# Optimization experiments

Measured on AMD Instinct MI355X. Metric: run time of the kernel, lower is better.

The kernel has to match this reference:

```python
import jax, jax.numpy as jnp
import numpy as np

N = 12288      # num nodes == in_num_dim (num_center_nodes)
D_IN = 512     # in_node_dim
D_EMB = 128    # embed_dim
D_OUT = 64     # out_dim
E = 393216     # num edges (avg degree 32)
NEG_SLOPE = 0.2  # GATConv default negative_slope


def _glorot(k, shape):
    lim = float(np.sqrt(6.0 / (shape[0] + shape[1])))
    return jax.random.uniform(k, shape, jnp.float32, -lim, lim)


def setup_inputs() -> dict:
    key = jax.random.key(0)
    ks = jax.random.split(key, 13)
    x = jax.random.normal(ks[0], (N, D_IN), jnp.float32)
    edge_index = jax.random.randint(ks[1], (2, E), 0, N, jnp.int64)
    # StructureAE.dense: Linear(in_node_dim, embed_dim)
    W_s1 = _glorot(ks[2], (D_EMB, D_IN))
    b_s1 = jnp.zeros((D_EMB,), jnp.float32)
    # GATConv(embed_dim, out_dim): heads=1, concat, bias
    W_g = _glorot(ks[3], (D_OUT, D_EMB))
    a_src = _glorot(ks[4], (D_OUT, 1))[:, 0]
    a_dst = _glorot(ks[5], (D_OUT, 1))[:, 0]
    b_g = jnp.zeros((D_OUT,), jnp.float32)
    # AttributeAE: dense1 = Linear(N, embed_dim), dense2 = Linear(embed_dim, out_dim)
    W_a1 = _glorot(ks[6], (D_EMB, N))
    b_a1 = jnp.zeros((D_EMB,), jnp.float32)
    W_a2 = _glorot(ks[7], (D_OUT, D_EMB))
    b_a2 = jnp.zeros((D_OUT,), jnp.float32)
    return dict(x=x, W_s1=W_s1, b_s1=b_s1, W_g=W_g, a_src=a_src, a_dst=a_dst,
                b_g=b_g, W_a1=W_a1, b_a1=b_a1, W_a2=W_a2, b_a2=b_a2,
                edge_index=edge_index, batch_size=N)


def _gat(x1, W_g, a_src, a_dst, b_g, edge_index):
    """Single-head GATConv with self-loops (PyG defaults)."""
    n = x1.shape[0]
    g = x1 @ W_g.T                                   # [N, D_OUT]
    loops = jnp.arange(n, dtype=edge_index.dtype)
    src = jnp.concatenate([edge_index[0], loops])    # message source j
    dst = jnp.concatenate([edge_index[1], loops])    # message target i
    sc_src = g @ a_src                               # [N]
    sc_dst = g @ a_dst                               # [N]
    e = jax.nn.leaky_relu(sc_src[src] + sc_dst[dst], NEG_SLOPE)  # [E+N]
    m = jax.ops.segment_max(e, dst, num_segments=n)
    e = jnp.exp(e - m[dst])
    denom = jax.ops.segment_sum(e, dst, num_segments=n)
    alpha = e / denom[dst]                           # softmax per target node
    h = jax.ops.segment_sum(alpha[:, None] * g[src], dst, num_segments=n)
    return h + b_g


def reference(x, W_s1, b_s1, W_g, a_src, a_dst, b_g,
              W_a1, b_a1, W_a2, b_a2, edge_index, batch_size):
    n = x.shape[0]
    # StructureAE (dropout=0 -> identity)
    x1 = jax.nn.relu(x @ W_s1.T + b_s1)              # [N, D_EMB]
    h = _gat(x1, W_g, a_src, a_dst, b_g, edge_index)  # [N, D_OUT]
    s_ = jax.nn.sigmoid(h @ h.T)                     # [N, N]
    # AttributeAE on x[:num_center_nodes] (pad if batch smaller)
    xp = x if batch_size >= n else jnp.pad(x, ((0, n - batch_size), (0, 0)))
    xt = jax.nn.relu(xp.T @ W_a1.T + b_a1)           # [D_IN, D_EMB]
    xa = xt @ W_a2.T + b_a2                          # [D_IN, D_OUT]
    x_ = h @ xa.T                                    # [N, D_IN]
    return (x_, s_)
```

## Files before the change

kernel.cpp:

```cpp
#include <hip/hip_runtime.h>
#include <cstddef>
#include <cstdint>

#define N_NODES 12288
#define D_IN    512
#define D_EMB   128
#define D_OUT   64
#define NEDGE   393216

typedef __attribute__((ext_vector_type(8))) short short8;
typedef __attribute__((ext_vector_type(4))) float f32x4;

__device__ __forceinline__ ushort f2bf(float f) {
  uint32_t u = __float_as_uint(f);
  u += 0x7fffu + ((u >> 16) & 1u);
  return (ushort)(u >> 16);
}
__device__ __forceinline__ float bf2f(ushort h) {
  return __uint_as_float((uint32_t)h << 16);
}

__global__ __launch_bounds__(256) void conv_hilo(const float* __restrict__ src,
    ushort* __restrict__ hi, ushort* __restrict__ lo)
{
  int idx = (blockIdx.x * 256 + threadIdx.x) * 4;
  float4 v = *(const float4*)(src + idx);
  const float* pv = &v.x;
  ushort4 h, l;
  ushort* ph = &h.x; ushort* pl = &l.x;
#pragma unroll
  for (int q = 0; q < 4; ++q) {
    ph[q] = f2bf(pv[q]);
    pl[q] = f2bf(pv[q] - bf2f(ph[q]));
  }
  *(ushort4*)(hi + idx) = h;
  *(ushort4*)(lo + idx) = l;
}

__global__ __launch_bounds__(256) void conv_x(const float* __restrict__ x,
    ushort* __restrict__ xhi, ushort* __restrict__ xlo,
    ushort* __restrict__ xThi, ushort* __restrict__ xTlo)
{
  __shared__ float t4[64][68];
  int i0 = blockIdx.x * 64, c0 = blockIdx.y * 64;
  int ty = threadIdx.x >> 2;
  int tx = threadIdx.x & 3;
#pragma unroll
  for (int p = 0; p < 4; ++p) {
    int col = (tx + p * 4) * 4;
    float4 v = *(const float4*)(x + (size_t)(i0 + ty) * D_IN + c0 + col);
    const float* pv = &v.x;
    ushort4 h, l;
    ushort* ph = &h.x; ushort* pl = &l.x;
#pragma unroll
    for (int q = 0; q < 4; ++q) {
      ph[q] = f2bf(pv[q]);
      pl[q] = f2bf(pv[q] - bf2f(ph[q]));
      t4[col + q][ty] = pv[q];
    }
    size_t o = (size_t)(i0 + ty) * D_IN + c0 + col;
    *(ushort4*)(xhi + o) = h;
    *(ushort4*)(xlo + o) = l;
  }
  __syncthreads();
  int cy = threadIdx.x >> 2;
  int cx = threadIdx.x & 3;
#pragma unroll
  for (int g4 = 0; g4 < 4; ++g4) {
    float4 w = *(const float4*)&t4[cy][cx * 16 + g4 * 4];
    const float* pw = &w.x;
    ushort4 th, tl;
    ushort* pth = &th.x; ushort* ptl = &tl.x;
#pragma unroll
    for (int q = 0; q < 4; ++q) {
      pth[q] = f2bf(pw[q]);
      ptl[q] = f2bf(pw[q] - bf2f(pth[q]));
    }
    size_t ot = (size_t)(c0 + cy) * N_NODES + i0 + cx * 16 + g4 * 4;
    *(ushort4*)(xThi + ot) = th;
    *(ushort4*)(xTlo + ot) = tl;
  }
}

__global__ __launch_bounds__(256) void init_kernel(const int* __restrict__ ei,
    int* __restrict__ flag, int* __restrict__ deg)
{
  int idx = blockIdx.x * 256 + threadIdx.x;
  if (idx < N_NODES) deg[idx] = 0;
  if (idx == 0) {
    int ok = 1;
    for (int t = 0; t < 64; ++t) ok &= (ei[2 * t + 1] == 0);
    *flag = ok;
  }
}

__global__ __launch_bounds__(256) void edge_deg(const int* __restrict__ ei,
    const int* __restrict__ flag, int* __restrict__ deg)
{
  int e = blockIdx.x * 256 + threadIdx.x;
  if (e >= NEDGE) return;
  int dst = (*flag) ? ei[2 * (NEDGE + e)] : ei[NEDGE + e];
  atomicAdd(&deg[dst], 1);
}

__global__ __launch_bounds__(256) void scan_deg(const int* __restrict__ deg,
    int* __restrict__ rp, int* __restrict__ cursor)
{
  __shared__ int sums[256];
  constexpr int C = N_NODES / 256;
  int t = threadIdx.x;
  int base = t * C;
  int local[C];
  int s = 0;
  for (int i = 0; i < C; ++i) { local[i] = deg[base + i]; s += local[i]; }
  sums[t] = s;
  __syncthreads();
  for (int off = 1; off < 256; off <<= 1) {
    int v = (t >= off) ? sums[t - off] : 0;
    __syncthreads();
    sums[t] += v;
    __syncthreads();
  }
  int prefix = (t == 0) ? 0 : sums[t - 1];
  for (int i = 0; i < C; ++i) {
    rp[base + i] = prefix;
    cursor[base + i] = prefix;
    prefix += local[i];
  }
  if (t == 255) rp[N_NODES] = prefix;
}

__global__ __launch_bounds__(256) void edge_scatter(const int* __restrict__ ei,
    const int* __restrict__ flag, int* __restrict__ cursor, int* __restrict__ csr)
{
  int e = blockIdx.x * 256 + threadIdx.x;
  if (e >= NEDGE) return;
  int is64 = *flag;
  int src = is64 ? ei[2 * e] : ei[e];
  int dst = is64 ? ei[2 * (NEDGE + e)] : ei[NEDGE + e];
  int p = atomicAdd(&cursor[dst], 1);
  csr[p] = src;
}

template<int WY, int WX, int MODE>
__global__ __launch_bounds__(256) void mfma_nt(
    const ushort* __restrict__ Ahi, const ushort* __restrict__ Alo,
    const ushort* __restrict__ Bhi, const ushort* __restrict__ Blo,
    const float* __restrict__ bias,
    float* __restrict__ Cf, ushort* __restrict__ Chi, ushort* __restrict__ Clo,
    int lda, int ldb, int K, int ldc, size_t part_stride)
{
  int lane = threadIdx.x & 63;
  int wave = threadIdx.x >> 6;
  int wy = wave / WX, wx = wave % WX;
  int i0 = blockIdx.x * (64 * WY) + wy * 64;
  int j0 = blockIdx.y * (64 * WX) + wx * 64;
  int kbase = blockIdx.z * K;
  float* Cout = Cf + (size_t)blockIdx.z * part_stride;
  int lm = lane & 15, lk = lane >> 4;
  f32x4 acc[4][4];
#pragma unroll
  for (int r = 0; r < 4; ++r)
#pragma unroll
    for (int c = 0; c < 4; ++c) acc[r][c] = (f32x4){0.f, 0.f, 0.f, 0.f};

  for (int k0 = 0; k0 < K; k0 += 32) {
    int kk = kbase + k0 + lk * 8;
    short8 Ah[4], Al[4], Bh[4], Bl[4];
#pragma unroll
    for (int t = 0; t < 4; ++t) {
      size_t ra = (size_t)(i0 + t * 16 + lm) * lda + kk;
      size_t rb = (size_t)(j0 + t * 16 + lm) * ldb + kk;
      Ah[t] = *(const short8*)(Ahi + ra);
      Al[t] = *(const short8*)(Alo + ra);
      Bh[t] = *(const short8*)(Bhi + rb);
      Bl[t] = *(const short8*)(Blo + rb);
    }
#pragma unroll
    for (int r = 0; r < 4; ++r)
#pragma unroll
      for (int c = 0; c < 4; ++c) {
        acc[r][c] = __builtin_amdgcn_mfma_f32_16x16x32_bf16(Ah[r], Bh[c], acc[r][c], 0, 0, 0);
        acc[r][c] = __builtin_amdgcn_mfma_f32_16x16x32_bf16(Ah[r], Bl[c], acc[r][c], 0, 0, 0);
        acc[r][c] = __builtin_amdgcn_mfma_f32_16x16x32_bf16(Al[r], Bh[c], acc[r][c], 0, 0, 0);
      }
  }
#pragma unroll
  for (int r = 0; r < 4; ++r)
#pragma unroll
    for (int c = 0; c < 4; ++c) {
      int col = j0 + c * 16 + lm;
#pragma unroll
      for (int q = 0; q < 4; ++q) {
        int row = i0 + r * 16 + lk * 4 + q;
        float v = acc[r][c][q];
        if (MODE == 0) {
          Cout[(size_t)row * ldc + col] = v;
        } else {
          v += bias[col];
          v = fmaxf(v, 0.f);
          ushort hb = f2bf(v);
          Chi[(size_t)row * ldc + col] = hb;
          Clo[(size_t)row * ldc + col] = f2bf(v - bf2f(hb));
        }
      }
    }
}

template<int ACT>
__global__ __launch_bounds__(256) void gemm_nt64(const float* __restrict__ A,
    const float* __restrict__ B, const float* __restrict__ bias,
    float* __restrict__ C, int M, int N, int K, int ldc)
{
  __shared__ float As[32][64];
  __shared__ float Bs[32][64];
  int m0 = blockIdx.x * 64, n0 = blockIdx.y * 64;
  int tid = threadIdx.x;
  int tx = tid & 15, ty = tid >> 4;
  float acc[4][4] = {};
  for (int k0 = 0; k0 < K; k0 += 32) {
#pragma unroll
    for (int p = 0; p < 2; ++p) {
      int idx = tid + p * 256;
      int row = idx >> 3;
      int kq  = idx & 7;
      float4 va = *(const float4*)(A + (size_t)(m0 + row) * K + k0 + kq * 4);
      As[kq*4+0][row] = va.x; As[kq*4+1][row] = va.y;
      As[kq*4+2][row] = va.z; As[kq*4+3][row] = va.w;
      float4 vb = *(const float4*)(B + (size_t)(n0 + row) * K + k0 + kq * 4);
      Bs[kq*4+0][row] = vb.x; Bs[kq*4+1][row] = vb.y;
      Bs[kq*4+2][row] = vb.z; Bs[kq*4+3][row] = vb.w;
    }
    __syncthreads();
#pragma unroll
    for (int k = 0; k < 32; ++k) {
      float a[4], b[4];
      *(float4*)a = *(const float4*)&As[k][ty * 4];
      *(float4*)b = *(const float4*)&Bs[k][tx * 4];
#pragma unroll
      for (int r = 0; r < 4; ++r)
#pragma unroll
        for (int c = 0; c < 4; ++c)
          acc[r][c] = fmaf(a[r], b[c], acc[r][c]);
    }
    __syncthreads();
  }
#pragma unroll
  for (int r = 0; r < 4; ++r) {
    int m = m0 + ty * 4 + r;
    float4 o;
    float* po = &o.x;
#pragma unroll
    for (int c = 0; c < 4; ++c) {
      float v = acc[r][c];
      if (bias) v += bias[n0 + tx * 4 + c];
      if (ACT) v = fmaxf(v, 0.f);
      po[c] = v;
    }
    *(float4*)(C + (size_t)m * ldc + n0 + tx * 4) = o;
  }
}

__global__ __launch_bounds__(256) void scores_kernel(const float* __restrict__ g,
    const float* __restrict__ a_src, const float* __restrict__ a_dst,
    float* __restrict__ sc_s, float* __restrict__ sc_d)
{
  int lane = threadIdx.x & 63;
  int i = blockIdx.x * 4 + (threadIdx.x >> 6);
  float gv = g[(size_t)i * 64 + lane];
  float vs = gv * a_src[lane];
  float vd = gv * a_dst[lane];
#pragma unroll
  for (int off = 32; off; off >>= 1) {
    vs += __shfl_xor(vs, off);
    vd += __shfl_xor(vd, off);
  }
  if (lane == 0) { sc_s[i] = vs; sc_d[i] = vd; }
}

__global__ __launch_bounds__(256) void gat_kernel(const int* __restrict__ rp,
    const int* __restrict__ csr, const float* __restrict__ sc_s,
    const float* __restrict__ sc_d, const float* __restrict__ g,
    const float* __restrict__ b_g,
    ushort* __restrict__ hhi, ushort* __restrict__ hlo)
{
  int lane = threadIdx.x & 63;
  int i = blockIdx.x * 4 + (threadIdx.x >> 6);
  int beg = rp[i], end = rp[i + 1];
  int deg = end - beg;
  float scd = sc_d[i];
  float mymax = -3.4e38f;
  for (int j = lane; j <= deg; j += 64) {
    int s = (j < deg) ? csr[beg + j] : i;
    float e = sc_s[s] + scd;
    e = (e > 0.f) ? e : 0.2f * e;
    mymax = fmaxf(mymax, e);
  }
#pragma unroll
  for (int off = 32; off; off >>= 1) mymax = fmaxf(mymax, __shfl_xor(mymax, off));
  float sum = 0.f;
  for (int j = lane; j <= deg; j += 64) {
    int s = (j < deg) ? csr[beg + j] : i;
    float e = sc_s[s] + scd;
    e = (e > 0.f) ? e : 0.2f * e;
    sum += __expf(e - mymax);
  }
#pragma unroll
  for (int off = 32; off; off >>= 1) sum += __shfl_xor(sum, off);
  float inv = 1.f / sum;
  float acc = 0.f;
  for (int j = 0; j <= deg; ++j) {
    int s = (j < deg) ? csr[beg + j] : i;
    float e = sc_s[s] + scd;
    e = (e > 0.f) ? e : 0.2f * e;
    float w = __expf(e - mymax) * inv;
    acc = fmaf(w, g[(size_t)s * 64 + lane], acc);
  }
  float val = acc + b_g[lane];
  size_t o = (size_t)i * 64 + lane;
  ushort hi = f2bf(val);
  hhi[o] = hi;
  hlo[o] = f2bf(val - bf2f(hi));
}

__global__ __launch_bounds__(256) void xt_ep(const float* __restrict__ part,
    const float* __restrict__ b_a1, float* __restrict__ xt)
{
  int idx = blockIdx.x * 256 + threadIdx.x;
  float v = b_a1[idx & 127];
#pragma unroll 8
  for (int c = 0; c < 32; ++c) v += part[(size_t)c * (D_IN * D_EMB) + idx];
  xt[idx] = fmaxf(v, 0.f);
}

__global__ __launch_bounds__(256) void sig_hht_mfma(const ushort* __restrict__ hhi,
    const ushort* __restrict__ hlo, float* __restrict__ out)
{
  int lane = threadIdx.x & 63;
  int wave = threadIdx.x >> 6;
  int i0 = blockIdx.x * 128 + (wave >> 1) * 64;
  int j0 = blockIdx.y * 128 + (wave & 1) * 64;
  int lm = lane & 15, lk = lane >> 4;
  f32x4 acc[4][4];
#pragma unroll
  for (int r = 0; r < 4; ++r)
#pragma unroll
    for (int c = 0; c < 4; ++c) acc[r][c] = (f32x4){0.f, 0.f, 0.f, 0.f};
#pragma unroll
  for (int ks = 0; ks < 2; ++ks) {
    short8 Ah[4], Al[4], Bh[4], Bl[4];
#pragma unroll
    for (int t = 0; t < 4; ++t) {
      size_t ra = (size_t)(i0 + t * 16 + lm) * 64 + ks * 32 + lk * 8;
      size_t rb = (size_t)(j0 + t * 16 + lm) * 64 + ks * 32 + lk * 8;
      Ah[t] = *(const short8*)(hhi + ra);
      Al[t] = *(const short8*)(hlo + ra);
      Bh[t] = *(const short8*)(hhi + rb);
      Bl[t] = *(const short8*)(hlo + rb);
    }
#pragma unroll
    for (int r = 0; r < 4; ++r)
#pragma unroll
      for (int c = 0; c < 4; ++c) {
        acc[r][c] = __builtin_amdgcn_mfma_f32_16x16x32_bf16(Ah[r], Bh[c], acc[r][c], 0, 0, 0);
        acc[r][c] = __builtin_amdgcn_mfma_f32_16x16x32_bf16(Ah[r], Bl[c], acc[r][c], 0, 0, 0);
        acc[r][c] = __builtin_amdgcn_mfma_f32_16x16x32_bf16(Al[r], Bh[c], acc[r][c], 0, 0, 0);
      }
  }
#pragma unroll
  for (int r = 0; r < 4; ++r)
#pragma unroll
    for (int c = 0; c < 4; ++c) {
#pragma unroll
      for (int q = 0; q < 4; ++q) {
        float v = acc[r][c][q];
        float ex = __expf(-v);
        float s = 1.f / (1.f + ex);
        out[(size_t)(i0 + r * 16 + lk * 4 + q) * N_NODES + (j0 + c * 16 + lm)] = s;
      }
    }
}

extern "C" void kernel_launch(void* const* d_in, const int* in_sizes, int n_in,
                              void* d_out, int out_size, void* d_ws, size_t ws_size,
                              hipStream_t stream)
{
  const float* x     = (const float*)d_in[0];
  const float* W_s1  = (const float*)d_in[1];
  const float* b_s1  = (const float*)d_in[2];
  const float* W_g   = (const float*)d_in[3];
  const float* a_src = (const float*)d_in[4];
  const float* a_dst = (const float*)d_in[5];
  const float* b_g   = (const float*)d_in[6];
  const float* W_a1  = (const float*)d_in[7];
  const float* b_a1  = (const float*)d_in[8];
  const float* W_a2  = (const float*)d_in[9];
  const float* b_a2  = (const float*)d_in[10];
  const int*   ei    = (const int*)d_in[11];

  float* ws   = (float*)d_ws;
  float* g    = ws;
  float* sc_s = g + (size_t)N_NODES * D_OUT;
  float* sc_d = sc_s + N_NODES;
  float* part = sc_d + N_NODES;
  float* xt   = part + (size_t)32 * D_IN * D_EMB;
  float* xa   = xt + D_IN * D_EMB;
  int* ip     = (int*)(xa + D_IN * D_OUT);
  int* flag   = ip;
  int* deg    = ip + 64;
  int* rp     = deg + N_NODES;
  int* cursor = rp + 12352;
  int* csr    = cursor + N_NODES;
  ushort* up  = (ushort*)(csr + NEDGE);
  ushort* xhi  = up;                         up += (size_t)N_NODES * D_IN;
  ushort* xlo  = up;                         up += (size_t)N_NODES * D_IN;
  ushort* xThi = up;                         up += (size_t)N_NODES * D_IN;
  ushort* xTlo = up;                         up += (size_t)N_NODES * D_IN;
  ushort* x1hi = up;                         up += (size_t)N_NODES * D_EMB;
  ushort* x1lo = up;                         up += (size_t)N_NODES * D_EMB;
  ushort* Ws1hi = up;                        up += (size_t)D_EMB * D_IN;
  ushort* Ws1lo = up;                        up += (size_t)D_EMB * D_IN;
  ushort* Wghi = up;                         up += (size_t)D_OUT * D_EMB;
  ushort* Wglo = up;                         up += (size_t)D_OUT * D_EMB;
  ushort* Wa1hi = up;                        up += (size_t)D_EMB * N_NODES;
  ushort* Wa1lo = up;                        up += (size_t)D_EMB * N_NODES;
  ushort* hhi = up;                          up += (size_t)N_NODES * D_OUT;
  ushort* hlo = up;                          up += (size_t)N_NODES * D_OUT;
  ushort* xahi = up;                         up += (size_t)D_IN * D_OUT;
  ushort* xalo = up;                         up += (size_t)D_IN * D_OUT;

  float* out_x = (float*)d_out;
  float* out_s = out_x + (size_t)N_NODES * D_IN;

  conv_x<<<dim3(192, 8), 256, 0, stream>>>(x, xhi, xlo, xThi, xTlo);
  conv_hilo<<<(D_EMB * D_IN) / 1024, 256, 0, stream>>>(W_s1, Ws1hi, Ws1lo);
  conv_hilo<<<(D_OUT * D_EMB) / 1024, 256, 0, stream>>>(W_g, Wghi, Wglo);
  conv_hilo<<<((size_t)D_EMB * N_NODES) / 1024, 256, 0, stream>>>(W_a1, Wa1hi, Wa1lo);

  init_kernel<<<48, 256, 0, stream>>>(ei, flag, deg);
  edge_deg<<<NEDGE / 256, 256, 0, stream>>>(ei, flag, deg);
  scan_deg<<<1, 256, 0, stream>>>(deg, rp, cursor);
  edge_scatter<<<NEDGE / 256, 256, 0, stream>>>(ei, flag, cursor, csr);

  mfma_nt<2, 2, 1><<<dim3(96, 1, 1), 256, 0, stream>>>(
      xhi, xlo, Ws1hi, Ws1lo, b_s1, nullptr, x1hi, x1lo,
      D_IN, D_IN, D_IN, D_EMB, 0);
  mfma_nt<4, 1, 0><<<dim3(48, 1, 1), 256, 0, stream>>>(
      x1hi, x1lo, Wghi, Wglo, nullptr, g, nullptr, nullptr,
      D_EMB, D_EMB, D_EMB, D_OUT, 0);
  scores_kernel<<<N_NODES / 4, 256, 0, stream>>>(g, a_src, a_dst, sc_s, sc_d);
  gat_kernel<<<N_NODES / 4, 256, 0, stream>>>(rp, csr, sc_s, sc_d, g, b_g,
                                              hhi, hlo);

  mfma_nt<2, 2, 0><<<dim3(4, 1, 32), 256, 0, stream>>>(
      xThi, xTlo, Wa1hi, Wa1lo, nullptr, part, nullptr, nullptr,
      N_NODES, N_NODES, 384, D_EMB, (size_t)D_IN * D_EMB);
  xt_ep<<<D_IN * D_EMB / 256, 256, 0, stream>>>(part, b_a1, xt);
  gemm_nt64<0><<<dim3(8, 1), 256, 0, stream>>>(xt, W_a2, b_a2, xa,
                                               D_IN, D_OUT, D_EMB, D_OUT);
  conv_hilo<<<(D_IN * D_OUT) / 1024, 256, 0, stream>>>(xa, xahi, xalo);

  mfma_nt<2, 2, 0><<<dim3(96, 4, 1), 256, 0, stream>>>(
      hhi, hlo, xahi, xalo, nullptr, out_x, nullptr, nullptr,
      D_OUT, D_OUT, D_OUT, D_IN, 0);
  sig_hht_mfma<<<dim3(96, 96), 256, 0, stream>>>(hhi, hlo, out_s);
}
```

Before: 969.5 us.

## Drop transposed x and W_a1 conversion, use FP32 split-K SIMT, cache GAT weights

Removes the transposed bf16 hi/lo copy of x and the hi/lo conversion of W_a1. The x^T·W_a1^T product is now computed directly from fp32 inputs with a shared-memory split-K SIMT kernel over 64 partitions, with a larger reduction in the epilogue. Small weight conversions are merged into one launch. The MFMA GEMMs switch to single-wave 64-thread blocks on a larger grid. The GAT kernel caches neighbor indices and exp weights in LDS so the third pass skips recomputation. The trade is less conversion traffic and fewer launches against slower non-MFMA FP32 arithmetic for the big reduction GEMM.

```diff
diff --git a/kernel.cpp b/kernel.cpp
--- a/kernel.cpp
+++ b/kernel.cpp
@@ -37,49 +37,25 @@
   *(ushort4*)(lo + idx) = l;
 }
 
-__global__ __launch_bounds__(256) void conv_x(const float* __restrict__ x,
-    ushort* __restrict__ xhi, ushort* __restrict__ xlo,
-    ushort* __restrict__ xThi, ushort* __restrict__ xTlo)
-{
-  __shared__ float t4[64][68];
-  int i0 = blockIdx.x * 64, c0 = blockIdx.y * 64;
-  int ty = threadIdx.x >> 2;
-  int tx = threadIdx.x & 3;
-#pragma unroll
-  for (int p = 0; p < 4; ++p) {
-    int col = (tx + p * 4) * 4;
-    float4 v = *(const float4*)(x + (size_t)(i0 + ty) * D_IN + c0 + col);
-    const float* pv = &v.x;
-    ushort4 h, l;
-    ushort* ph = &h.x; ushort* pl = &l.x;
-#pragma unroll
-    for (int q = 0; q < 4; ++q) {
-      ph[q] = f2bf(pv[q]);
-      pl[q] = f2bf(pv[q] - bf2f(ph[q]));
-      t4[col + q][ty] = pv[q];
-    }
-    size_t o = (size_t)(i0 + ty) * D_IN + c0 + col;
-    *(ushort4*)(xhi + o) = h;
-    *(ushort4*)(xlo + o) = l;
-  }
-  __syncthreads();
-  int cy = threadIdx.x >> 2;
-  int cx = threadIdx.x & 3;
-#pragma unroll
-  for (int g4 = 0; g4 < 4; ++g4) {
-    float4 w = *(const float4*)&t4[cy][cx * 16 + g4 * 4];
-    const float* pw = &w.x;
-    ushort4 th, tl;
-    ushort* pth = &th.x; ushort* ptl = &tl.x;
-#pragma unroll
-    for (int q = 0; q < 4; ++q) {
-      pth[q] = f2bf(pw[q]);
-      ptl[q] = f2bf(pw[q] - bf2f(pth[q]));
-    }
-    size_t ot = (size_t)(c0 + cy) * N_NODES + i0 + cx * 16 + g4 * 4;
-    *(ushort4*)(xThi + ot) = th;
-    *(ushort4*)(xTlo + ot) = tl;
-  }
+__global__ __launch_bounds__(256) void conv_w(const float* __restrict__ Ws1,
+    const float* __restrict__ Wg, ushort* __restrict__ s1h, ushort* __restrict__ s1l,
+    ushort* __restrict__ wgh, ushort* __restrict__ wgl)
+{
+  int b = blockIdx.x;
+  const float* src; ushort* hi; ushort* lo; int idx;
+  if (b < 64) { src = Ws1; hi = s1h; lo = s1l; idx = (b * 256 + threadIdx.x) * 4; }
+  else        { src = Wg;  hi = wgh; lo = wgl; idx = ((b - 64) * 256 + threadIdx.x) * 4; }
+  float4 v = *(const float4*)(src + idx);
+  const float* pv = &v.x;
+  ushort4 h, l;
+  ushort* ph = &h.x; ushort* pl = &l.x;
+#pragma unroll
+  for (int q = 0; q < 4; ++q) {
+    ph[q] = f2bf(pv[q]);
+    pl[q] = f2bf(pv[q] - bf2f(ph[q]));
+  }
+  *(ushort4*)(hi + idx) = h;
+  *(ushort4*)(lo + idx) = l;
 }
 
 __global__ __launch_bounds__(256) void init_kernel(const int* __restrict__ ei,
@@ -142,21 +118,17 @@
   csr[p] = src;
 }
 
-template<int WY, int WX, int MODE>
-__global__ __launch_bounds__(256) void mfma_nt(
+template<int MODE>
+__global__ __launch_bounds__(64) void mfma_nt1(
     const ushort* __restrict__ Ahi, const ushort* __restrict__ Alo,
     const ushort* __restrict__ Bhi, const ushort* __restrict__ Blo,
     const float* __restrict__ bias,
     float* __restrict__ Cf, ushort* __restrict__ Chi, ushort* __restrict__ Clo,
-    int lda, int ldb, int K, int ldc, size_t part_stride)
-{
-  int lane = threadIdx.x & 63;
-  int wave = threadIdx.x >> 6;
-  int wy = wave / WX, wx = wave % WX;
-  int i0 = blockIdx.x * (64 * WY) + wy * 64;
-  int j0 = blockIdx.y * (64 * WX) + wx * 64;
-  int kbase = blockIdx.z * K;
-  float* Cout = Cf + (size_t)blockIdx.z * part_stride;
+    int lda, int ldb, int K, int ldc)
+{
+  int lane = threadIdx.x;
+  int i0 = blockIdx.x * 64;
+  int j0 = blockIdx.y * 64;
   int lm = lane & 15, lk = lane >> 4;
   f32x4 acc[4][4];
 #pragma unroll
@@ -165,7 +137,7 @@
     for (int c = 0; c < 4; ++c) acc[r][c] = (f32x4){0.f, 0.f, 0.f, 0.f};
 
   for (int k0 = 0; k0 < K; k0 += 32) {
-    int kk = kbase + k0 + lk * 8;
+    int kk = k0 + lk * 8;
     short8 Ah[4], Al[4], Bh[4], Bl[4];
 #pragma unroll
     for (int t = 0; t < 4; ++t) {
@@ -195,7 +167,7 @@
         int row = i0 + r * 16 + lk * 4 + q;
         float v = acc[r][c][q];
         if (MODE == 0) {
-          Cout[(size_t)row * ldc + col] = v;
+          Cf[(size_t)row * ldc + col] = v;
         } else {
           v += bias[col];
           v = fmaxf(v, 0.f);
@@ -278,14 +250,18 @@
   if (lane == 0) { sc_s[i] = vs; sc_d[i] = vd; }
 }
 
+#define WCAP 192
 __global__ __launch_bounds__(256) void gat_kernel(const int* __restrict__ rp,
     const int* __restrict__ csr, const float* __restrict__ sc_s,
     const float* __restrict__ sc_d, const float* __restrict__ g,
     const float* __restrict__ b_g,
     ushort* __restrict__ hhi, ushort* __restrict__ hlo)
 {
+  __shared__ float wbuf[4][WCAP];
+  __shared__ int   sbuf[4][WCAP];
   int lane = threadIdx.x & 63;
-  int i = blockIdx.x * 4 + (threadIdx.x >> 6);
+  int w = threadIdx.x >> 6;
+  int i = blockIdx.x * 4 + w;
   int beg = rp[i], end = rp[i + 1];
   int deg = end - beg;
   float scd = sc_d[i];
@@ -295,26 +271,33 @@
     float e = sc_s[s] + scd;
     e = (e > 0.f) ? e : 0.2f * e;
     mymax = fmaxf(mymax, e);
+    if (j < WCAP) sbuf[w][j] = s;
   }
 #pragma unroll
   for (int off = 32; off; off >>= 1) mymax = fmaxf(mymax, __shfl_xor(mymax, off));
   float sum = 0.f;
   for (int j = lane; j <= deg; j += 64) {
-    int s = (j < deg) ? csr[beg + j] : i;
+    int s = (j < WCAP) ? sbuf[w][j] : ((j < deg) ? csr[beg + j] : i);
     float e = sc_s[s] + scd;
     e = (e > 0.f) ? e : 0.2f * e;
-    sum += __expf(e - mymax);
+    float ex = __expf(e - mymax);
+    sum += ex;
+    if (j < WCAP) wbuf[w][j] = ex;
   }
 #pragma unroll
   for (int off = 32; off; off >>= 1) sum += __shfl_xor(sum, off);
   float inv = 1.f / sum;
   float acc = 0.f;
   for (int j = 0; j <= deg; ++j) {
-    int s = (j < deg) ? csr[beg + j] : i;
-    float e = sc_s[s] + scd;
-    e = (e > 0.f) ? e : 0.2f * e;
-    float w = __expf(e - mymax) * inv;
-    acc = fmaf(w, g[(size_t)s * 64 + lane], acc);
+    int s; float ex;
+    if (j < WCAP) { s = sbuf[w][j]; ex = wbuf[w][j]; }
+    else {
+      s = (j < deg) ? csr[beg + j] : i;
+      float e = sc_s[s] + scd;
+      e = (e > 0.f) ? e : 0.2f * e;
+      ex = __expf(e - mymax);
+    }
+    acc = fmaf(ex * inv, g[(size_t)s * 64 + lane], acc);
   }
   float val = acc + b_g[lane];
   size_t o = (size_t)i * 64 + lane;
@@ -323,13 +306,66 @@
   hlo[o] = f2bf(val - bf2f(hi));
 }
 
+__global__ __launch_bounds__(256) void xt_splitk(const float* __restrict__ x,
+    const float* __restrict__ Wa1, float* __restrict__ part)
+{
+  __shared__ float Xs[32][64];
+  __shared__ float Ws[32][128];
+  int c0 = blockIdx.x * 64;
+  int i0 = blockIdx.y * 192;
+  float* pout = part + (size_t)blockIdx.y * (D_IN * D_EMB);
+  int tid = threadIdx.x;
+  int txc = tid & 15, txj = tid >> 4;
+  float acc[4][8] = {};
+  for (int ib = 0; ib < 192; ib += 32) {
+#pragma unroll
+    for (int p = 0; p < 2; ++p) {
+      int idx = tid + p * 256;
+      int row = idx >> 4, q = idx & 15;
+      *(float4*)&Xs[row][q * 4] =
+          *(const float4*)(x + (size_t)(i0 + ib + row) * D_IN + c0 + q * 4);
+    }
+#pragma unroll
+    for (int p = 0; p < 4; ++p) {
+      int idx = tid + p * 256;
+      int j = idx >> 3, q = idx & 7;
+      float4 v = *(const float4*)(Wa1 + (size_t)j * N_NODES + i0 + ib + q * 4);
+      Ws[q*4+0][j] = v.x; Ws[q*4+1][j] = v.y;
+      Ws[q*4+2][j] = v.z; Ws[q*4+3][j] = v.w;
+    }
+    __syncthreads();
+#pragma unroll
+    for (int ii = 0; ii < 32; ++ii) {
+      float a[4], b[8];
+      *(float4*)a = *(const float4*)&Xs[ii][txc * 4];
+      *(float4*)&b[0] = *(const float4*)&Ws[ii][txj * 8];
+      *(float4*)&b[4] = *(const float4*)&Ws[ii][txj * 8 + 4];
+#pragma unroll
+      for (int r = 0; r < 4; ++r)
+#pragma unroll
+        for (int c = 0; c < 8; ++c)
+          acc[r][c] = fmaf(a[r], b[c], acc[r][c]);
+    }
+    __syncthreads();
+  }
+#pragma unroll
+  for (int r = 0; r < 4; ++r) {
+    float4 o0, o1;
+    o0.x = acc[r][0]; o0.y = acc[r][1]; o0.z = acc[r][2]; o0.w = acc[r][3];
+    o1.x = acc[r][4]; o1.y = acc[r][5]; o1.z = acc[r][6]; o1.w = acc[r][7];
+    size_t off = (size_t)(c0 + txc * 4 + r) * D_EMB + txj * 8;
+    *(float4*)&pout[off] = o0;
+    *(float4*)&pout[off + 4] = o1;
+  }
+}
+
 __global__ __launch_bounds__(256) void xt_ep(const float* __restrict__ part,
     const float* __restrict__ b_a1, float* __restrict__ xt)
 {
   int idx = blockIdx.x * 256 + threadIdx.x;
   float v = b_a1[idx & 127];
 #pragma unroll 8
-  for (int c = 0; c < 32; ++c) v += part[(size_t)c * (D_IN * D_EMB) + idx];
+  for (int c = 0; c < 64; ++c) v += part[(size_t)c * (D_IN * D_EMB) + idx];
   xt[idx] = fmaxf(v, 0.f);
 }
 
@@ -403,7 +439,7 @@
   float* sc_s = g + (size_t)N_NODES * D_OUT;
   float* sc_d = sc_s + N_NODES;
   float* part = sc_d + N_NODES;
-  float* xt   = part + (size_t)32 * D_IN * D_EMB;
+  float* xt   = part + (size_t)64 * D_IN * D_EMB;
   float* xa   = xt + D_IN * D_EMB;
   int* ip     = (int*)(xa + D_IN * D_OUT);
   int* flag   = ip;
@@ -414,16 +450,12 @@
   ushort* up  = (ushort*)(csr + NEDGE);
   ushort* xhi  = up;                         up += (size_t)N_NODES * D_IN;
   ushort* xlo  = up;                         up += (size_t)N_NODES * D_IN;
-  ushort* xThi = up;                         up += (size_t)N_NODES * D_IN;
-  ushort* xTlo = up;                         up += (size_t)N_NODES * D_IN;
   ushort* x1hi = up;                         up += (size_t)N_NODES * D_EMB;
   ushort* x1lo = up;                         up += (size_t)N_NODES * D_EMB;
   ushort* Ws1hi = up;                        up += (size_t)D_EMB * D_IN;
   ushort* Ws1lo = up;                        up += (size_t)D_EMB * D_IN;
   ushort* Wghi = up;                         up += (size_t)D_OUT * D_EMB;
   ushort* Wglo = up;                         up += (size_t)D_OUT * D_EMB;
-  ushort* Wa1hi = up;                        up += (size_t)D_EMB * N_NODES;
-  ushort* Wa1lo = up;                        up += (size_t)D_EMB * N_NODES;
   ushort* hhi = up;                          up += (size_t)N_NODES * D_OUT;
   ushort* hlo = up;                          up += (size_t)N_NODES * D_OUT;
   ushort* xahi = up;                         up += (size_t)D_IN * D_OUT;
@@ -432,36 +464,32 @@
   float* out_x = (float*)d_out;
   float* out_s = out_x + (size_t)N_NODES * D_IN;
 
-  conv_x<<<dim3(192, 8), 256, 0, stream>>>(x, xhi, xlo, xThi, xTlo);
-  conv_hilo<<<(D_EMB * D_IN) / 1024, 256, 0, stream>>>(W_s1, Ws1hi, Ws1lo);
-  conv_hilo<<<(D_OUT * D_EMB) / 1024, 256, 0, stream>>>(W_g, Wghi, Wglo);
-  conv_hilo<<<((size_t)D_EMB * N_NODES) / 1024, 256, 0, stream>>>(W_a1, Wa1hi, Wa1lo);
+  conv_hilo<<<(N_NODES * D_IN) / 1024, 256, 0, stream>>>(x, xhi, xlo);
+  conv_w<<<72, 256, 0, stream>>>(W_s1, W_g, Ws1hi, Ws1lo, Wghi, Wglo);
 
   init_kernel<<<48, 256, 0, stream>>>(ei, flag, deg);
   edge_deg<<<NEDGE / 256, 256, 0, stream>>>(ei, flag, deg);
   scan_deg<<<1, 256, 0, stream>>>(deg, rp, cursor);
   edge_scatter<<<NEDGE / 256, 256, 0, stream>>>(ei, flag, cursor, csr);
 
-  mfma_nt<2, 2, 1><<<dim3(96, 1, 1), 256, 0, stream>>>(
+  mfma_nt1<1><<<dim3(192, 2), 64, 0, stream>>>(
       xhi, xlo, Ws1hi, Ws1lo, b_s1, nullptr, x1hi, x1lo,
-      D_IN, D_IN, D_IN, D_EMB, 0);
-  mfma_nt<4, 1, 0><<<dim3(48, 1, 1), 256, 0, stream>>>(
+      D_IN, D_IN, D_IN, D_EMB);
+  mfma_nt1<0><<<dim3(192, 1), 64, 0, stream>>>(
       x1hi, x1lo, Wghi, Wglo, nullptr, g, nullptr, nullptr,
-      D_EMB, D_EMB, D_EMB, D_OUT, 0);
+      D_EMB, D_EMB, D_EMB, D_OUT);
   scores_kernel<<<N_NODES / 4, 256, 0, stream>>>(g, a_src, a_dst, sc_s, sc_d);
   gat_kernel<<<N_NODES / 4, 256, 0, stream>>>(rp, csr, sc_s, sc_d, g, b_g,
                                               hhi, hlo);
 
-  mfma_nt<2, 2, 0><<<dim3(4, 1, 32), 256, 0, stream>>>(
-      xThi, xTlo, Wa1hi, Wa1lo, nullptr, part, nullptr, nullptr,
-      N_NODES, N_NODES, 384, D_EMB, (size_t)D_IN * D_EMB);
+  xt_splitk<<<dim3(8, 64), 256, 0, stream>>>(x, W_a1, part);
   xt_ep<<<D_IN * D_EMB / 256, 256, 0, stream>>>(part, b_a1, xt);
   gemm_nt64<0><<<dim3(8, 1), 256, 0, stream>>>(xt, W_a2, b_a2, xa,
                                                D_IN, D_OUT, D_EMB, D_OUT);
   conv_hilo<<<(D_IN * D_OUT) / 1024, 256, 0, stream>>>(xa, xahi, xalo);
 
-  mfma_nt<2, 2, 0><<<dim3(96, 4, 1), 256, 0, stream>>>(
+  mfma_nt1<0><<<dim3(192, 8), 64, 0, stream>>>(
       hhi, hlo, xahi, xalo, nullptr, out_x, nullptr, nullptr,
-      D_OUT, D_OUT, D_OUT, D_IN, 0);
+      D_OUT, D_OUT, D_OUT, D_IN);
   sig_hht_mfma<<<dim3(96, 96), 256, 0, stream>>>(hhi, hlo, out_s);
 }
```

Measured after the change: 914.6 us. -5.7%, faster.
